# Kernel tuning notes

Hardware: AMD Instinct MI355X
Metric: run time of the kernel (lower is better)

The kernel has to match this reference:

```python
import jax, jax.numpy as jnp
import numpy as np

H = 512
W = 512
N_STROKES = 5000
S = 10          # samples_per_curve
K = 20          # strokes_per_pixel
CANVAS_COLOR = 0.5  # 'gray'
COARSE = 5      # coarse grid downsample factor (H//5, W//5)


def setup_inputs() -> dict:
    key = jax.random.key(0)
    ks = jax.random.split(key, 6)
    # stroke centers spread over the canvas
    location = jax.random.uniform(ks[0], (N_STROKES, 2), jnp.float32) * jnp.array([H, W], jnp.float32)
    # bezier control-point offsets relative to the stroke center
    curve_s = jax.random.normal(ks[1], (N_STROKES, 2), jnp.float32) * 8.0
    curve_e = jax.random.normal(ks[2], (N_STROKES, 2), jnp.float32) * 8.0
    curve_c = jax.random.normal(ks[3], (N_STROKES, 2), jnp.float32) * 8.0
    color = jax.random.uniform(ks[4], (N_STROKES, 3), jnp.float32)
    width = jax.random.uniform(ks[5], (N_STROKES, 1), jnp.float32) * 4.0 + 1.0
    return {"curve_s": curve_s, "curve_e": curve_e, "curve_c": curve_c,
            "color": color, "location": location, "width": width}


def _bezier_points(s, c, e, num_points):
    # s, c, e: [N, 2] -> [N, num_points, 2]
    t = jnp.linspace(0.0, 1.0, num_points).astype(jnp.float32)  # [S]
    omt2 = (1.0 - t) ** 2  # [S]
    t2 = t ** 2
    # x/y computed identically: c + (1-t)^2 (s - c) + t^2 (e - c)
    pts = c[:, None, :] + omt2[None, :, None] * (s - c)[:, None, :] \
          + t2[None, :, None] * (e - c)[:, None, :]
    return pts  # [N, S, 2]


def _nearest_upsample_idx(out_size, in_size):
    # torch F.interpolate mode='nearest': src = floor(dst * in/out)
    idx = jnp.floor(jnp.arange(out_size) * (in_size / out_size)).astype(jnp.int32)
    return jnp.clip(idx, 0, in_size - 1)


def reference(curve_s, curve_e, curve_c, color, location, width):
    # sample bezier curve points (absolute coords)
    pts = _bezier_points(curve_s + location, curve_c + location,
                         curve_e + location, S)  # [N, S, 2]

    # ---- coarse-grid KNN over stroke centers ----
    Hc, Wc = H // COARSE, W // COARSE
    tH = jnp.linspace(0.0, float(H), Hc).astype(jnp.float32)
    tW = jnp.linspace(0.0, float(W), Wc).astype(jnp.float32)
    Px, Py = jnp.meshgrid(tH, tW, indexing='ij')
    P = jnp.stack([Px, Py], axis=-1)  # [Hc, Wc, 2]
    D_centers = jnp.sum(jnp.square(P[:, :, None, :] - location), axis=-1)  # [Hc, Wc, N]
    _, idcs = jax.lax.top_k(-D_centers, K)  # [Hc, Wc, K]

    near_pts = pts[idcs]      # [Hc, Wc, K, S, 2]
    near_col = color[idcs]    # [Hc, Wc, K, 3]
    near_w = width[idcs]      # [Hc, Wc, K, 1]

    # ---- upsample coarse gathers to full res ----
    ih = _nearest_upsample_idx(H, Hc)
    iw = _nearest_upsample_idx(W, Wc)
    near_pts = near_pts[ih][:, iw]   # [H, W, K, S, 2] (nearest)
    near_col = near_col[ih][:, iw]   # [H, W, K, 3]   (nearest)
    # widths: bilinear (align_corners=False, no antialias) per channel
    near_w = jax.image.resize(near_w[..., 0], (H, W, K), method='linear')[..., None]  # [H, W, K, 1]

    # ---- full-res pixel grid ----
    tHf = jnp.linspace(0.0, float(H), H).astype(jnp.float32)
    tWf = jnp.linspace(0.0, float(W), W).astype(jnp.float32)
    Pxf, Pyf = jnp.meshgrid(tHf, tWf, indexing='ij')
    P_full = jnp.stack([Pxf, Pyf], axis=-1)  # [H, W, 2]

    # ---- per-pixel closest point on each polyline segment ----
    a = near_pts[:, :, :, :S - 1, :]              # [H, W, K, S-1, 2]
    b_a = near_pts[:, :, :, 1:, :] - a            # segment direction
    pa = P_full[:, :, None, None, :] - a          # pixel - segment start
    t = jnp.sum(b_a * pa, axis=-1) / jnp.sum(jnp.square(b_a), axis=-1)
    t = jnp.clip(t, 0.0, 1.0)
    closest = a + t[..., None] * b_a
    dist = jnp.sum(jnp.square(P_full[:, :, None, None, :] - closest), axis=-1)  # [H, W, K, S-1]

    D = jnp.min(dist, axis=(-1, -2))  # [H, W]
    min_per_stroke = jnp.min(dist, axis=-1)  # [H, W, K]
    ranking = jax.nn.softmax(100000.0 * (1.0 / (1e-08 + min_per_stroke)), axis=-1)  # [H, W, K]

    I_colors = jnp.einsum('hwkf,hwk->hwf', near_col, ranking)  # [H, W, 3]
    bs = jnp.einsum('hwkf,hwk->hwf', near_w, ranking)          # [H, W, 1]
    bs_mask = jax.nn.sigmoid(bs - D[..., None])
    canvas = jnp.full_like(I_colors, CANVAS_COLOR)
    I = I_colors * bs_mask + (1.0 - bs_mask) * canvas
    return I
```

## Files before the change

### kernel.cpp

```cpp
#include <hip/hip_runtime.h>
#include <math.h>

#define NS 5000
#define SS 10
#define KK 20
#define HC 102
#define NBIN 32
#define BINW 16.0f
#define CAP 192

#define WAVE_SYNC() __asm__ volatile("s_waitcnt lgkmcnt(0)" ::: "memory")

__global__ void prep_kernel(const float* __restrict__ cs, const float* __restrict__ ce,
                            const float* __restrict__ cc, const float* __restrict__ loc,
                            const float* __restrict__ color, const float* __restrict__ width,
                            float* __restrict__ sdata, float4* __restrict__ ctab,
                            int* __restrict__ binCnt) {
    int i = blockIdx.x * 256 + threadIdx.x;
    if (i >= NS) return;
    float lx = loc[i*2+0], ly = loc[i*2+1];
    float sx = cs[i*2+0] + lx, sy = cs[i*2+1] + ly;
    float ex = ce[i*2+0] + lx, ey = ce[i*2+1] + ly;
    float px = cc[i*2+0] + lx, py = cc[i*2+1] + ly;
    float qx[SS], qy[SS];
    #pragma unroll
    for (int j = 0; j < SS; ++j) {
        float t = (float)j * (1.0f / 9.0f);
        float omt = 1.0f - t;
        float omt2 = omt * omt, t2 = t * t;
        qx[j] = px + omt2 * (sx - px) + t2 * (ex - px);
        qy[j] = py + omt2 * (sy - py) + t2 * (ey - py);
        sdata[i*32 + 2*j + 0] = qx[j];
        sdata[i*32 + 2*j + 1] = qy[j];
    }
    #pragma unroll
    for (int sg = 0; sg < 9; ++sg) {
        float bx = qx[sg+1] - qx[sg], by = qy[sg+1] - qy[sg];
        sdata[i*32 + 20 + sg] = 1.0f / (bx*bx + by*by);
    }
    sdata[i*32 + 29] = 0.0f; sdata[i*32 + 30] = 0.0f; sdata[i*32 + 31] = 0.0f;
    ctab[i] = make_float4(color[i*3+0], color[i*3+1], color[i*3+2], width[i]);
    int b0 = min(max((int)(lx * (1.0f/BINW)), 0), NBIN-1);
    int b1 = min(max((int)(ly * (1.0f/BINW)), 0), NBIN-1);
    atomicAdd(&binCnt[b0*NBIN + b1], 1);
}

__global__ void binscan_kernel(const int* __restrict__ binCnt, int* __restrict__ binStart) {
    __shared__ int wsum[4];
    int t = threadIdx.x;
    int lane = t & 63, w = t >> 6;
    int4 v = ((const int4*)binCnt)[t];
    int s0 = v.x, s1 = s0 + v.y, s2 = s1 + v.z, s3 = s2 + v.w;
    int x = s3;
    #pragma unroll
    for (int off = 1; off < 64; off <<= 1) {
        int y = __shfl_up(x, off, 64);
        if (lane >= off) x += y;
    }
    if (lane == 63) wsum[w] = x;
    __syncthreads();
    int woff = 0;
    #pragma unroll
    for (int i = 0; i < 4; ++i) woff += (i < w) ? wsum[i] : 0;
    int texcl = woff + x - s3;
    binStart[4*t+1] = texcl + s0;
    binStart[4*t+2] = texcl + s1;
    binStart[4*t+3] = texcl + s2;
    binStart[4*t+4] = texcl + s3;
    if (t == 0) binStart[0] = 0;
}

__global__ void binscatter_kernel(const float* __restrict__ loc, const int* __restrict__ binStart,
                                  int* __restrict__ binFill, float2* __restrict__ sxy,
                                  int* __restrict__ sid) {
    int i = blockIdx.x * 256 + threadIdx.x;
    if (i >= NS) return;
    float l0 = loc[i*2+0], l1 = loc[i*2+1];
    int b0 = min(max((int)(l0 * (1.0f/BINW)), 0), NBIN-1);
    int b1 = min(max((int)(l1 * (1.0f/BINW)), 0), NBIN-1);
    int b = b0*NBIN + b1;
    int pos = binStart[b] + atomicAdd(&binFill[b], 1);
    sxy[pos] = make_float2(l0, l1);
    sid[pos] = i;
}

__global__ void __launch_bounds__(256) topk_kernel(const float* __restrict__ loc,
                                                   const float* __restrict__ width,
                                                   const float2* __restrict__ sxy,
                                                   const int* __restrict__ sid,
                                                   const int* __restrict__ binStart,
                                                   int* __restrict__ idcs,
                                                   float* __restrict__ wk) {
    __shared__ unsigned long long sk[4][CAP];
    int w = threadIdx.x >> 6, lane = threadIdx.x & 63;
    int cell = blockIdx.x * 4 + w;
    int ci = cell / HC, cj = cell - ci * HC;
    const float dc = 512.0f / 101.0f;
    float c0 = (float)ci * dc;
    float c1 = (float)cj * dc;
    unsigned long long below = (1ull << lane) - 1ull;

    float R = 30.0f;
    int cnt = 0;
    for (int attempt = 0; attempt < 5; ++attempt) {
        float R2 = R * R;
        int base = 0;
        int by0 = max((int)((c0 - R) * (1.0f/BINW)), 0);
        int by1 = min((int)((c0 + R) * (1.0f/BINW)), NBIN-1);
        int bx0 = max((int)((c1 - R) * (1.0f/BINW)), 0);
        int bx1 = min((int)((c1 + R) * (1.0f/BINW)), NBIN-1);
        for (int by = by0; by <= by1; ++by) {
            int s = binStart[by*NBIN + bx0];
            int e = binStart[by*NBIN + bx1 + 1];
            for (int t0 = s; t0 < e; t0 += 64) {
                int t = t0 + lane;
                int tc = min(t, e - 1);
                float2 p = sxy[tc];
                float dx = c0 - p.x, dy = c1 - p.y;
                float d = dx*dx + dy*dy;
                bool pred = (t < e) && (d < R2);
                unsigned long long mask = __ballot(pred);
                int pos = base + __popcll(mask & below);
                if (pred && pos < CAP)
                    sk[w][pos] = ((unsigned long long)__float_as_uint(d) << 32)
                               | (unsigned int)sid[tc];
                base += __popcll(mask);
            }
        }
        cnt = base;
        if (cnt >= KK) break;
        R *= 1.6f;
    }
    WAVE_SYNC();

    if (cnt >= KK && cnt <= CAP) {
        if (cnt <= 64) {
            unsigned long long k0 = (lane < cnt) ? sk[w][lane] : ~0ull;
            int r0 = 0;
            int j = 0;
            #pragma unroll 1
            for (; j + 4 <= cnt; j += 4) {
                unsigned long long a = sk[w][j],   b = sk[w][j+1];
                unsigned long long c = sk[w][j+2], d = sk[w][j+3];
                r0 += (int)(a < k0) + (int)(b < k0) + (int)(c < k0) + (int)(d < k0);
            }
            for (; j < cnt; ++j) r0 += (int)(sk[w][j] < k0);
            if (r0 < KK && lane < cnt) {
                int idx = (int)(unsigned int)(k0 & 0xffffffffull);
                idcs[cell*KK + r0] = idx;
                wk[cell*KK + r0]   = width[idx];
            }
        } else {
            unsigned long long k0 = (lane       < cnt) ? sk[w][lane]       : ~0ull;
            unsigned long long k1 = (lane + 64  < cnt) ? sk[w][lane + 64]  : ~0ull;
            unsigned long long k2 = (lane + 128 < cnt) ? sk[w][lane + 128] : ~0ull;
            int r0 = 0, r1 = 0, r2 = 0;
            #pragma unroll 1
            for (int j = 0; j < cnt; ++j) {
                unsigned long long a = sk[w][j];
                r0 += (int)(a < k0); r1 += (int)(a < k1); r2 += (int)(a < k2);
            }
            if (r0 < KK && lane < cnt) {
                int idx = (int)(unsigned int)(k0 & 0xffffffffull);
                idcs[cell*KK + r0] = idx;  wk[cell*KK + r0] = width[idx];
            }
            if (r1 < KK && lane + 64 < cnt) {
                int idx = (int)(unsigned int)(k1 & 0xffffffffull);
                idcs[cell*KK + r1] = idx;  wk[cell*KK + r1] = width[idx];
            }
            if (r2 < KK && lane + 128 < cnt) {
                int idx = (int)(unsigned int)(k2 & 0xffffffffull);
                idcs[cell*KK + r2] = idx;  wk[cell*KK + r2] = width[idx];
            }
        }
    } else {
        if (lane == 0) {
            float bd[KK]; int bi[KK];
            for (int k = 0; k < KK; ++k) { bd[k] = 3.4e38f; bi[k] = 0; }
            for (int n = 0; n < NS; ++n) {
                float dx = c0 - loc[n*2+0];
                float dy = c1 - loc[n*2+1];
                float d = dx*dx + dy*dy;
                if (d < bd[KK-1]) {
                    int p = KK - 1;
                    while (p > 0 && bd[p-1] > d) { bd[p] = bd[p-1]; bi[p] = bi[p-1]; --p; }
                    bd[p] = d; bi[p] = n;
                }
            }
            for (int k = 0; k < KK; ++k) {
                idcs[cell*KK + k] = bi[k];
                wk[cell*KK + k]   = width[bi[k]];
            }
        }
    }
}

__global__ void __launch_bounds__(256, 4) render_kernel(const float* __restrict__ sdata,
                                                        const float4* __restrict__ ctab,
                                                        const int* __restrict__ idcs,
                                                        const float* __restrict__ wk,
                                                        float* __restrict__ out) {
    int x = blockIdx.x * 64 + threadIdx.x;
    int y = blockIdx.y * 4  + threadIdx.y;
    const float df = 512.0f / 511.0f;
    float p0 = (float)y * df;
    float p1 = (float)x * df;
    int cy = (y * 51) >> 8;
    int cx = (x * 51) >> 8;

    const int4* mip = (const int4*)(idcs + (cy * HC + cx) * KK);
    int4 m0 = mip[0], m1 = mip[1], m2 = mip[2], m3 = mip[3], m4 = mip[4];
    int idxs[KK] = {m0.x,m0.y,m0.z,m0.w, m1.x,m1.y,m1.z,m1.w, m2.x,m2.y,m2.z,m2.w,
                    m3.x,m3.y,m3.z,m3.w, m4.x,m4.y,m4.z,m4.w};

    const float sc = 102.0f / 512.0f;
    float iny = ((float)y + 0.5f) * sc - 0.5f;
    float inx = ((float)x + 0.5f) * sc - 0.5f;
    float y0f = floorf(iny), x0f = floorf(inx);
    float fy = iny - y0f, fx = inx - x0f;
    int y0 = min(max((int)y0f, 0), HC - 1);
    int y1 = min(max((int)y0f + 1, 0), HC - 1);
    int x0 = min(max((int)x0f, 0), HC - 1);
    int x1 = min(max((int)x0f + 1, 0), HC - 1);
    const float* w00 = wk + (y0 * HC + x0) * KK;
    const float* w01 = wk + (y0 * HC + x1) * KK;
    const float* w10 = wk + (y1 * HC + x0) * KK;
    const float* w11 = wk + (y1 * HC + x1) * KK;

    float m = -INFINITY, s = 0.0f;
    float a0 = 0.0f, a1 = 0.0f, a2 = 0.0f, wa = 0.0f;
    float D = INFINITY;

    #pragma unroll 4
    for (int k = 0; k < KK; ++k) {
        int idx = idxs[k];
        const float4* sp = (const float4*)(sdata + idx * 32);
        float4 f0 = sp[0], f1 = sp[1], f2 = sp[2], f3 = sp[3], f4 = sp[4];
        float4 i0 = sp[5], i1 = sp[6], i2 = sp[7];
        float4 cw = ctab[idx];
        float qx[10] = {f0.x, f0.z, f1.x, f1.z, f2.x, f2.z, f3.x, f3.z, f4.x, f4.z};
        float qy[10] = {f0.y, f0.w, f1.y, f1.w, f2.y, f2.w, f3.y, f3.w, f4.y, f4.w};
        float iv[9]  = {i0.x, i0.y, i0.z, i0.w, i1.x, i1.y, i1.z, i1.w, i2.x};
        float mink = INFINITY;
        #pragma unroll
        for (int sg = 0; sg < 9; ++sg) {
            float ax = qx[sg], ay = qy[sg];
            float bx = qx[sg+1] - ax, by = qy[sg+1] - ay;
            float pax = p0 - ax, pay = p1 - ay;
            float dot = bx * pax + by * pay;
            float t = dot * iv[sg];
            t = fminf(fmaxf(t, 0.0f), 1.0f);
            float ccx = ax + t * bx, ccy = ay + t * by;
            float ddx = p0 - ccx, ddy = p1 - ccy;
            float d = ddx * ddx + ddy * ddy;
            mink = fminf(mink, d);
        }
        D = fminf(D, mink);
        float z = 100000.0f / (1e-8f + mink);
        float wkv = (1.0f - fy) * ((1.0f - fx) * w00[k] + fx * w01[k])
                  +          fy * ((1.0f - fx) * w10[k] + fx * w11[k]);
        float nm  = fmaxf(m, z);
        float scl = __expf(m - nm);
        float e   = __expf(z - nm);
        s  = s  * scl + e;
        a0 = a0 * scl + cw.x * e;
        a1 = a1 * scl + cw.y * e;
        a2 = a2 * scl + cw.z * e;
        wa = wa * scl + wkv  * e;
        m = nm;
    }
    float inv = 1.0f / s;
    float bs = wa * inv;
    float msk = 1.0f / (1.0f + __expf(-(bs - D)));
    float o0 = a0 * inv * msk + (1.0f - msk) * 0.5f;
    float o1 = a1 * inv * msk + (1.0f - msk) * 0.5f;
    float o2 = a2 * inv * msk + (1.0f - msk) * 0.5f;
    int base = (y * 512 + x) * 3;
    out[base+0] = o0;
    out[base+1] = o1;
    out[base+2] = o2;
}

extern "C" void kernel_launch(void* const* d_in, const int* in_sizes, int n_in,
                              void* d_out, int out_size, void* d_ws, size_t ws_size,
                              hipStream_t stream) {
    const float* cs    = (const float*)d_in[0];
    const float* ce    = (const float*)d_in[1];
    const float* cc    = (const float*)d_in[2];
    const float* color = (const float*)d_in[3];
    const float* loc   = (const float*)d_in[4];
    const float* width = (const float*)d_in[5];
    float* out = (float*)d_out;

    char* p = (char*)d_ws;
    float*  sdata    = (float*)p;                 p += NS * 32 * sizeof(float);
    float4* ctab     = (float4*)p;                p += NS * sizeof(float4);
    int*    idcs     = (int*)p;                   p += (size_t)HC*HC*KK*sizeof(int);
    float*  wk       = (float*)p;                 p += (size_t)HC*HC*KK*sizeof(float);
    int*    binCnt   = (int*)p;                   p += NBIN*NBIN*sizeof(int);
    int*    binFill  = (int*)p;                   p += NBIN*NBIN*sizeof(int);
    int*    binStart = (int*)p;                   p += 4112;
    float2* sxy      = (float2*)p;                p += NS * sizeof(float2);
    int*    sid      = (int*)p;

    hipMemsetAsync(binCnt, 0, 2 * NBIN * NBIN * sizeof(int), stream);

    prep_kernel      <<<(NS + 255) / 256, 256, 0, stream>>>(cs, ce, cc, loc, color, width,
                                                            sdata, ctab, binCnt);
    binscan_kernel   <<<1, 256, 0, stream>>>(binCnt, binStart);
    binscatter_kernel<<<(NS + 255) / 256, 256, 0, stream>>>(loc, binStart, binFill, sxy, sid);
    topk_kernel      <<<(HC*HC)/4, 256, 0, stream>>>(loc, width, sxy, sid, binStart, idcs, wk);
    render_kernel    <<<dim3(512/64, 512/4), dim3(64, 4), 0, stream>>>(sdata, ctab, idcs, wk, out);
}
```

Baseline: 134.5 us.

## Fuse prep, bin scan and scatter into one block; prefetch strokes in render

Merges the stroke preparation, bin histogram, prefix scan and scatter into a single 1024-thread workgroup kernel that uses shared-memory atomics. This removes a memset and two kernel launches along with the global atomics between them. The render loop now software-prefetches the next stroke's data while the current stroke is processed, and its unrolling is disabled. The cost is that the prep work runs on only one CU, and the bin order inside each bin stays nondeterministic.

```diff
diff --git a/kernel.cpp b/kernel.cpp
--- a/kernel.cpp
+++ b/kernel.cpp
@@ -11,47 +11,50 @@
 
 #define WAVE_SYNC() __asm__ volatile("s_waitcnt lgkmcnt(0)" ::: "memory")
 
-__global__ void prep_kernel(const float* __restrict__ cs, const float* __restrict__ ce,
-                            const float* __restrict__ cc, const float* __restrict__ loc,
-                            const float* __restrict__ color, const float* __restrict__ width,
-                            float* __restrict__ sdata, float4* __restrict__ ctab,
-                            int* __restrict__ binCnt) {
-    int i = blockIdx.x * 256 + threadIdx.x;
-    if (i >= NS) return;
-    float lx = loc[i*2+0], ly = loc[i*2+1];
-    float sx = cs[i*2+0] + lx, sy = cs[i*2+1] + ly;
-    float ex = ce[i*2+0] + lx, ey = ce[i*2+1] + ly;
-    float px = cc[i*2+0] + lx, py = cc[i*2+1] + ly;
-    float qx[SS], qy[SS];
-    #pragma unroll
-    for (int j = 0; j < SS; ++j) {
-        float t = (float)j * (1.0f / 9.0f);
-        float omt = 1.0f - t;
-        float omt2 = omt * omt, t2 = t * t;
-        qx[j] = px + omt2 * (sx - px) + t2 * (ex - px);
-        qy[j] = py + omt2 * (sy - py) + t2 * (ey - py);
-        sdata[i*32 + 2*j + 0] = qx[j];
-        sdata[i*32 + 2*j + 1] = qy[j];
-    }
-    #pragma unroll
-    for (int sg = 0; sg < 9; ++sg) {
-        float bx = qx[sg+1] - qx[sg], by = qy[sg+1] - qy[sg];
-        sdata[i*32 + 20 + sg] = 1.0f / (bx*bx + by*by);
-    }
-    sdata[i*32 + 29] = 0.0f; sdata[i*32 + 30] = 0.0f; sdata[i*32 + 31] = 0.0f;
-    ctab[i] = make_float4(color[i*3+0], color[i*3+1], color[i*3+2], width[i]);
-    int b0 = min(max((int)(lx * (1.0f/BINW)), 0), NBIN-1);
-    int b1 = min(max((int)(ly * (1.0f/BINW)), 0), NBIN-1);
-    atomicAdd(&binCnt[b0*NBIN + b1], 1);
-}
-
-__global__ void binscan_kernel(const int* __restrict__ binCnt, int* __restrict__ binStart) {
-    __shared__ int wsum[4];
+__global__ void __launch_bounds__(1024) build_kernel(
+        const float* __restrict__ cs, const float* __restrict__ ce,
+        const float* __restrict__ cc, const float* __restrict__ loc,
+        const float* __restrict__ color, const float* __restrict__ width,
+        float* __restrict__ sdata, float4* __restrict__ ctab,
+        int* __restrict__ binStart, float2* __restrict__ sxy, int* __restrict__ sid) {
+    __shared__ int cnt[NBIN*NBIN];
+    __shared__ int wsum[16];
     int t = threadIdx.x;
+    cnt[t] = 0;
+    __syncthreads();
+
+    for (int i = t; i < NS; i += 1024) {
+        float lx = loc[i*2+0], ly = loc[i*2+1];
+        float sx = cs[i*2+0] + lx, sy = cs[i*2+1] + ly;
+        float ex = ce[i*2+0] + lx, ey = ce[i*2+1] + ly;
+        float px = cc[i*2+0] + lx, py = cc[i*2+1] + ly;
+        float qx[SS], qy[SS];
+        #pragma unroll
+        for (int j = 0; j < SS; ++j) {
+            float tt = (float)j * (1.0f / 9.0f);
+            float omt = 1.0f - tt;
+            float omt2 = omt * omt, t2 = tt * tt;
+            qx[j] = px + omt2 * (sx - px) + t2 * (ex - px);
+            qy[j] = py + omt2 * (sy - py) + t2 * (ey - py);
+            sdata[i*32 + 2*j + 0] = qx[j];
+            sdata[i*32 + 2*j + 1] = qy[j];
+        }
+        #pragma unroll
+        for (int sg = 0; sg < 9; ++sg) {
+            float bx = qx[sg+1] - qx[sg], by = qy[sg+1] - qy[sg];
+            sdata[i*32 + 20 + sg] = 1.0f / (bx*bx + by*by);
+        }
+        sdata[i*32 + 29] = 0.0f; sdata[i*32 + 30] = 0.0f; sdata[i*32 + 31] = 0.0f;
+        ctab[i] = make_float4(color[i*3+0], color[i*3+1], color[i*3+2], width[i]);
+        int b0 = min(max((int)(lx * (1.0f/BINW)), 0), NBIN-1);
+        int b1 = min(max((int)(ly * (1.0f/BINW)), 0), NBIN-1);
+        atomicAdd(&cnt[b0*NBIN + b1], 1);
+    }
+    __syncthreads();
+
+    int v = cnt[t];
     int lane = t & 63, w = t >> 6;
-    int4 v = ((const int4*)binCnt)[t];
-    int s0 = v.x, s1 = s0 + v.y, s2 = s1 + v.z, s3 = s2 + v.w;
-    int x = s3;
+    int x = v;
     #pragma unroll
     for (int off = 1; off < 64; off <<= 1) {
         int y = __shfl_up(x, off, 64);
@@ -61,27 +64,21 @@
     __syncthreads();
     int woff = 0;
     #pragma unroll
-    for (int i = 0; i < 4; ++i) woff += (i < w) ? wsum[i] : 0;
-    int texcl = woff + x - s3;
-    binStart[4*t+1] = texcl + s0;
-    binStart[4*t+2] = texcl + s1;
-    binStart[4*t+3] = texcl + s2;
-    binStart[4*t+4] = texcl + s3;
+    for (int i = 0; i < 16; ++i) woff += (i < w) ? wsum[i] : 0;
+    int incl = woff + x;
+    cnt[t] = incl - v;
+    binStart[t + 1] = incl;
     if (t == 0) binStart[0] = 0;
-}
-
-__global__ void binscatter_kernel(const float* __restrict__ loc, const int* __restrict__ binStart,
-                                  int* __restrict__ binFill, float2* __restrict__ sxy,
-                                  int* __restrict__ sid) {
-    int i = blockIdx.x * 256 + threadIdx.x;
-    if (i >= NS) return;
-    float l0 = loc[i*2+0], l1 = loc[i*2+1];
-    int b0 = min(max((int)(l0 * (1.0f/BINW)), 0), NBIN-1);
-    int b1 = min(max((int)(l1 * (1.0f/BINW)), 0), NBIN-1);
-    int b = b0*NBIN + b1;
-    int pos = binStart[b] + atomicAdd(&binFill[b], 1);
-    sxy[pos] = make_float2(l0, l1);
-    sid[pos] = i;
+    __syncthreads();
+
+    for (int i = t; i < NS; i += 1024) {
+        float l0 = loc[i*2+0], l1 = loc[i*2+1];
+        int b0 = min(max((int)(l0 * (1.0f/BINW)), 0), NBIN-1);
+        int b1 = min(max((int)(l1 * (1.0f/BINW)), 0), NBIN-1);
+        int pos = atomicAdd(&cnt[b0*NBIN + b1], 1);
+        sxy[pos] = make_float2(l0, l1);
+        sid[pos] = i;
+    }
 }
 
 __global__ void __launch_bounds__(256) topk_kernel(const float* __restrict__ loc,
@@ -231,13 +228,22 @@
     float a0 = 0.0f, a1 = 0.0f, a2 = 0.0f, wa = 0.0f;
     float D = INFINITY;
 
-    #pragma unroll 4
+    const float4* sp = (const float4*)(sdata + idxs[0] * 32);
+    float4 nf0 = sp[0], nf1 = sp[1], nf2 = sp[2], nf3 = sp[3], nf4 = sp[4];
+    float4 ni0 = sp[5], ni1 = sp[6], ni2 = sp[7];
+    float4 ncw = ctab[idxs[0]];
+
+    #pragma unroll 1
     for (int k = 0; k < KK; ++k) {
-        int idx = idxs[k];
-        const float4* sp = (const float4*)(sdata + idx * 32);
-        float4 f0 = sp[0], f1 = sp[1], f2 = sp[2], f3 = sp[3], f4 = sp[4];
-        float4 i0 = sp[5], i1 = sp[6], i2 = sp[7];
-        float4 cw = ctab[idx];
+        float4 f0 = nf0, f1 = nf1, f2 = nf2, f3 = nf3, f4 = nf4;
+        float4 i0 = ni0, i1 = ni1, i2 = ni2;
+        float4 cw = ncw;
+        if (k + 1 < KK) {
+            const float4* spn = (const float4*)(sdata + idxs[k+1] * 32);
+            nf0 = spn[0]; nf1 = spn[1]; nf2 = spn[2]; nf3 = spn[3]; nf4 = spn[4];
+            ni0 = spn[5]; ni1 = spn[6]; ni2 = spn[7];
+            ncw = ctab[idxs[k+1]];
+        }
         float qx[10] = {f0.x, f0.z, f1.x, f1.z, f2.x, f2.z, f3.x, f3.z, f4.x, f4.z};
         float qy[10] = {f0.y, f0.w, f1.y, f1.w, f2.y, f2.w, f3.y, f3.w, f4.y, f4.w};
         float iv[9]  = {i0.x, i0.y, i0.z, i0.w, i1.x, i1.y, i1.z, i1.w, i2.x};
@@ -297,18 +303,12 @@
     float4* ctab     = (float4*)p;                p += NS * sizeof(float4);
     int*    idcs     = (int*)p;                   p += (size_t)HC*HC*KK*sizeof(int);
     float*  wk       = (float*)p;                 p += (size_t)HC*HC*KK*sizeof(float);
-    int*    binCnt   = (int*)p;                   p += NBIN*NBIN*sizeof(int);
-    int*    binFill  = (int*)p;                   p += NBIN*NBIN*sizeof(int);
     int*    binStart = (int*)p;                   p += 4112;
     float2* sxy      = (float2*)p;                p += NS * sizeof(float2);
     int*    sid      = (int*)p;
 
-    hipMemsetAsync(binCnt, 0, 2 * NBIN * NBIN * sizeof(int), stream);
-
-    prep_kernel      <<<(NS + 255) / 256, 256, 0, stream>>>(cs, ce, cc, loc, color, width,
-                                                            sdata, ctab, binCnt);
-    binscan_kernel   <<<1, 256, 0, stream>>>(binCnt, binStart);
-    binscatter_kernel<<<(NS + 255) / 256, 256, 0, stream>>>(loc, binStart, binFill, sxy, sid);
-    topk_kernel      <<<(HC*HC)/4, 256, 0, stream>>>(loc, width, sxy, sid, binStart, idcs, wk);
-    render_kernel    <<<dim3(512/64, 512/4), dim3(64, 4), 0, stream>>>(sdata, ctab, idcs, wk, out);
+    build_kernel <<<1, 1024, 0, stream>>>(cs, ce, cc, loc, color, width,
+                                          sdata, ctab, binStart, sxy, sid);
+    topk_kernel  <<<(HC*HC)/4, 256, 0, stream>>>(loc, width, sxy, sid, binStart, idcs, wk);
+    render_kernel<<<dim3(512/64, 512/4), dim3(64, 4), 0, stream>>>(sdata, ctab, idcs, wk, out);
 }
```

Result: slower. 172.4 us (+28.2%).
